# Optimization experiments

Measured on AMD Instinct MI355X. Metric: run time of the kernel, lower is better.

## Reference

```python
import jax, jax.numpy as jnp
import numpy as np

H = 4   # num_heads
D = 32  # out_dim per head
NEG_SLOPE = 0.01  # torch F.leaky_relu default


def setup_inputs() -> dict:
    key = jax.random.key(0)
    ks = jax.random.split(key, 8)
    N, E, IN, ED = 50000, 600000, 128, 64
    node_feats = jax.random.normal(ks[0], (N, IN), dtype=jnp.float32)
    edge_feats = jax.random.normal(ks[1], (E, ED), dtype=jnp.float32)
    src = jax.random.randint(ks[2], (E,), 0, N, dtype=jnp.int32)
    dst = jax.random.randint(ks[3], (E,), 0, N, dtype=jnp.int32)
    # Xavier-ish scaled weights to keep softmax logits sane
    Wn = jax.random.normal(ks[4], (IN, H * D), dtype=jnp.float32) * (1.0 / np.sqrt(IN))
    We = jax.random.normal(ks[5], (ED, H * D), dtype=jnp.float32) * (1.0 / np.sqrt(ED))
    Wa = jax.random.normal(ks[6], (2 * D,), dtype=jnp.float32) * (1.0 / np.sqrt(2 * D))
    Wo = jax.random.normal(ks[7], (H * D, D), dtype=jnp.float32) * (1.0 / np.sqrt(H * D))
    return {"node_feats": node_feats, "edge_feats": edge_feats, "src": src,
            "dst": dst, "Wn": Wn, "We": We, "Wa": Wa, "Wo": Wo}


def reference(node_feats, edge_feats, src, dst, Wn, We, Wa, Wo):
    N = node_feats.shape[0]
    # projections -> [N,H,D] and [E,H,D]
    zn = (node_feats @ Wn).reshape(N, H, D)
    ze = (edge_feats @ We).reshape(-1, H, D)
    # edge attention logits: concat([z_src+z_e, z_dst+z_e]) @ Wa, leaky_relu
    zs = zn[src] + ze                              # [E,H,D]
    zd = zn[dst] + ze                              # [E,H,D]
    e = jnp.einsum('ehd,d->eh', zs, Wa[:D]) + jnp.einsum('ehd,d->eh', zd, Wa[D:])
    e = jax.nn.leaky_relu(e, NEG_SLOPE)            # [E,H]
    # segment softmax over incoming edges of each destination node
    emax = jax.ops.segment_max(e, dst, num_segments=N)       # [N,H]
    emax = jnp.where(jnp.isfinite(emax), emax, 0.0)          # empty segments
    ex = jnp.exp(e - emax[dst])                              # [E,H]
    denom = jax.ops.segment_sum(ex, dst, num_segments=N)     # [N,H]
    alpha = ex / denom[dst]                                  # [E,H]
    # weighted scatter-sum of edge messages
    agg = jax.ops.segment_sum(alpha[..., None] * ze, dst, num_segments=N)  # [N,H,D]
    # DGL update_all leaves zero-in-degree nodes with their projected feats
    deg = jax.ops.segment_sum(jnp.ones_like(dst, dtype=jnp.float32), dst, num_segments=N)
    z = jnp.where((deg > 0)[:, None, None], agg, zn)
    out = jax.nn.relu(z.reshape(N, H * D) @ Wo)   # activation=relu; dropout is identity in eval
    return out
```

## Files before the change

### kernel.cpp

```cpp
#include <hip/hip_runtime.h>
#include <hip/hip_fp16.h>
#include <math.h>

#define HH 4
#define DD 32
#define HD 128
#define INF 128
#define EDF 64
#define NEG 0.01f
#define NB 256
#define CHUNK 64
#define GS_LOGIT 1024
#define GS_AGG   2048
#define GS_NODES 1024

template <int CTRL>
__device__ __forceinline__ float dpp_add(float v) {
    int t = __builtin_amdgcn_update_dpp(0, __float_as_int(v), CTRL, 0xF, 0xF, true);
    return v + __int_as_float(t);
}
__device__ __forceinline__ float red16(float v) {
    v = dpp_add<0xB1>(v);
    v = dpp_add<0x4E>(v);
    v = dpp_add<0x141>(v);
    v = dpp_add<0x140>(v);
    return v;
}

__global__ void k_pre(const float* __restrict__ Wn, const float* __restrict__ We,
                      const float* __restrict__ Wa, const float* __restrict__ Wo,
                      float* __restrict__ WnA, float* __restrict__ WnB,
                      float* __restrict__ WeC, float* __restrict__ WeWo,
                      float* __restrict__ WnWo, int* __restrict__ deg, int N) {
    int b = blockIdx.x, tid = threadIdx.x;
    if (b >= 25) {
        int i = (b - 25) * 512 + tid;
        if (i < N) deg[i] = 0;
        return;
    }
    if (b < 16) {
        int t = b * 512 + tid;
        int j = t >> 5, o = t & 31;
        int h = j >> 6, k = j & 63;
        float a = 0.f;
        for (int d = 0; d < DD; ++d)
            a += We[k * HD + h * DD + d] * Wo[(h * DD + d) * DD + o];
        WeWo[t] = a;
    } else if (b < 24) {
        int u = (b - 16) * 512 + tid;
        int k = u >> 5, o = u & 31;
        float a = 0.f;
        for (int d = 0; d < HD; ++d)
            a += Wn[k * HD + d] * Wo[d * DD + o];
        WnWo[u] = a;
    } else {
        int k = tid >> 2, h = tid & 3;
        float a = 0.f, bb = 0.f;
        for (int d = 0; d < DD; ++d) {
            float w = Wn[k * HD + h * DD + d];
            a += w * Wa[d];
            bb += w * Wa[DD + d];
        }
        WnA[k * HH + h] = a;
        WnB[k * HH + h] = bb;
        if (k < EDF) {
            float c = 0.f;
            for (int d = 0; d < DD; ++d)
                c += We[k * HD + h * DD + d] * (Wa[d] + Wa[DD + d]);
            WeC[k * HH + h] = c;
        }
    }
}

__global__ void k_nodes(const float* __restrict__ X, const float* __restrict__ WnA,
                        const float* __restrict__ WnB, float* __restrict__ an,
                        float* __restrict__ bn, int N) {
    int wave = threadIdx.x >> 6, lane = threadIdx.x & 63;
    int stride = gridDim.x * 4;
    for (int n = blockIdx.x * 4 + wave; n < N; n += stride) {
        float x0 = X[(size_t)n * INF + lane];
        float x1 = X[(size_t)n * INF + 64 + lane];
        float pa[HH], pb[HH];
#pragma unroll
        for (int h = 0; h < HH; ++h) {
            pa[h] = x0 * WnA[lane * HH + h] + x1 * WnA[(lane + 64) * HH + h];
            pb[h] = x0 * WnB[lane * HH + h] + x1 * WnB[(lane + 64) * HH + h];
        }
#pragma unroll
        for (int off = 32; off; off >>= 1)
#pragma unroll
            for (int h = 0; h < HH; ++h) {
                pa[h] += __shfl_xor(pa[h], off);
                pb[h] += __shfl_xor(pb[h], off);
            }
        if (lane == 0)
#pragma unroll
            for (int h = 0; h < HH; ++h) {
                an[(size_t)n * HH + h] = pa[h];
                bn[(size_t)n * HH + h] = pb[h];
            }
    }
}

__global__ void k_hist(const int* __restrict__ dst, int* __restrict__ deg,
                       int* __restrict__ rank, int E) {
    int e = blockIdx.x * blockDim.x + threadIdx.x;
    if (e < E) rank[e] = atomicAdd(&deg[dst[e]], 1);
}
__global__ void k_scan1(const int* __restrict__ deg, int* __restrict__ partial,
                        int N, int chunk) {
    __shared__ int s[256];
    int tid = threadIdx.x;
    int i = blockIdx.x * chunk + tid;
    int v = (tid < chunk && i < N) ? deg[i] : 0;
    s[tid] = v; __syncthreads();
    for (int off = 128; off; off >>= 1) {
        if (tid < off) s[tid] += s[tid + off];
        __syncthreads();
    }
    if (tid == 0) partial[blockIdx.x] = s[0];
}
__global__ void k_scan2(const int* __restrict__ partial, int* __restrict__ pscan) {
    __shared__ int s[NB];
    int tid = threadIdx.x;
    int v = partial[tid];
    s[tid] = v; __syncthreads();
    for (int off = 1; off < NB; off <<= 1) {
        int t = (tid >= off) ? s[tid - off] : 0;
        __syncthreads();
        s[tid] += t;
        __syncthreads();
    }
    pscan[tid] = s[tid] - v;
}
__global__ void k_scan3(const int* __restrict__ deg, const int* __restrict__ pscan,
                        int* __restrict__ offs, int2* __restrict__ nd,
                        int N, int chunk) {
    __shared__ int s[256];
    int tid = threadIdx.x;
    int i = blockIdx.x * chunk + tid;
    int v = (tid < chunk && i < N) ? deg[i] : 0;
    s[tid] = v; __syncthreads();
    for (int off = 1; off < 256; off <<= 1) {
        int t = (tid >= off) ? s[tid - off] : 0;
        __syncthreads();
        s[tid] += t;
        __syncthreads();
    }
    if (tid < chunk && i < N) {
        int o = pscan[blockIdx.x] + s[tid] - v;
        offs[i] = o;
        nd[i] = make_int2(o, v);
    }
}
__global__ void k_perm(const int* __restrict__ dst, const int* __restrict__ offs,
                       const int* __restrict__ rank, int* __restrict__ eids,
                       int* __restrict__ pos_of, int E) {
    int e = blockIdx.x * blockDim.x + threadIdx.x;
    if (e < E) {
        int p = offs[dst[e]] + rank[e];
        pos_of[e] = p;
        eids[p] = e;
    }
}

struct Quad { float4 x; int s, d, p, e; bool v; };

__device__ __forceinline__ Quad loadq(const float* __restrict__ EF,
                                      const int* __restrict__ src,
                                      const int* __restrict__ dst,
                                      const int* __restrict__ pos_of,
                                      int idx, int nq, int g, int q, int E) {
    Quad r;
    int qi = idx < nq ? idx : nq - 1;
    int e = qi * 4 + g;
    r.v = (idx < nq) && (e < E);
    if (e >= E) e = E - 1;
    r.e = e;
    r.x = *(const float4*)(EF + (size_t)e * EDF + q * 4);
    r.s = src[e];
    r.d = dst[e];
    r.p = pos_of[e];
    return r;
}

__global__ void k_logit(const float* __restrict__ EF, const float* __restrict__ an,
                        const float* __restrict__ bn, const float* __restrict__ WeC,
                        const int* __restrict__ src, const int* __restrict__ dst,
                        const int* __restrict__ pos_of,
                        float* __restrict__ wep, __half* __restrict__ EF16, int E) {
    int wave = threadIdx.x >> 6, lane = threadIdx.x & 63;
    int g = lane >> 4, q = lane & 15;
    float4 c0 = *(const float4*)(WeC + (q * 4 + 0) * 4);
    float4 c1 = *(const float4*)(WeC + (q * 4 + 1) * 4);
    float4 c2 = *(const float4*)(WeC + (q * 4 + 2) * 4);
    float4 c3 = *(const float4*)(WeC + (q * 4 + 3) * 4);
    int nq = (E + 3) >> 2;
    int stride = gridDim.x * 4;
    int i0 = blockIdx.x * 4 + wave;
    if (i0 >= nq) return;
    Quad A = loadq(EF, src, dst, pos_of, i0, nq, g, q, E);
    Quad B = loadq(EF, src, dst, pos_of, i0 + stride, nq, g, q, E);
    float4 anA = *(const float4*)(an + (size_t)A.s * HH);
    float4 bnA = *(const float4*)(bn + (size_t)A.d * HH);
    for (int i = i0; i < nq; i += stride) {
        Quad C = loadq(EF, src, dst, pos_of, i + 2 * stride, nq, g, q, E);
        float4 anB = *(const float4*)(an + (size_t)B.s * HH);
        float4 bnB = *(const float4*)(bn + (size_t)B.d * HH);
        float ae0 = red16(A.x.x * c0.x + A.x.y * c1.x + A.x.z * c2.x + A.x.w * c3.x);
        float ae1 = red16(A.x.x * c0.y + A.x.y * c1.y + A.x.z * c2.y + A.x.w * c3.y);
        float ae2 = red16(A.x.x * c0.z + A.x.y * c1.z + A.x.z * c2.z + A.x.w * c3.z);
        float ae3 = red16(A.x.x * c0.w + A.x.y * c1.w + A.x.z * c2.w + A.x.w * c3.w);
        if (A.v) {
            __half2 h01 = __floats2half2_rn(A.x.x, A.x.y);
            __half2 h23 = __floats2half2_rn(A.x.z, A.x.w);
            __half2* hp = (__half2*)(EF16 + (size_t)A.e * EDF + q * 4);
            hp[0] = h01;
            hp[1] = h23;
            if (q == 0) {
                float l0 = anA.x + bnA.x + ae0;
                float l1 = anA.y + bnA.y + ae1;
                float l2 = anA.z + bnA.z + ae2;
                float l3 = anA.w + bnA.w + ae3;
                float4 w4;
                w4.x = __expf(l0 > 0.f ? l0 : NEG * l0);
                w4.y = __expf(l1 > 0.f ? l1 : NEG * l1);
                w4.z = __expf(l2 > 0.f ? l2 : NEG * l2);
                w4.w = __expf(l3 > 0.f ? l3 : NEG * l3);
                *(float4*)(wep + (size_t)A.p * 4) = w4;
            }
        }
        A = B; anA = anB; bnA = bnB;
        B = C;
    }
}

__global__ void k_agg(const __half* __restrict__ EF16, const float* __restrict__ wep,
                      const int* __restrict__ eids, const int2* __restrict__ nd,
                      const float* __restrict__ WW, const float* __restrict__ X,
                      const float* __restrict__ WnWo, float* __restrict__ out, int N) {
    __shared__ float ww_s[256 * 32];
    __shared__ float smem[4][264];
    __shared__ int   ebuf[4][CHUNK];
    for (int i = threadIdx.x; i < 256 * 32; i += 256)
        ww_s[i] = WW[i];
    __syncthreads();

    int wave = threadIdx.x >> 6, lane = threadIdx.x & 63;
    int s8 = lane >> 3, o4 = lane & 7;
    int stride = gridDim.x * 4;
    for (int n = blockIdx.x * 4 + wave; n < N; n += stride) {
        int2 sd = nd[n];
        int st = sd.x, dn = sd.y;
        if (dn == 0) {
            if (lane < 32) {
                float a = 0.f;
                for (int k = 0; k < INF; ++k)
                    a += X[(size_t)n * INF + k] * WnWo[k * DD + lane];
                out[(size_t)n * DD + lane] = fmaxf(a, 0.f);
            }
            continue;
        }
        float4* wbuf = (float4*)smem[wave];
        const __half* base = EF16 + lane;
        float gacc[4] = {0.f, 0.f, 0.f, 0.f};
        float den[4]  = {0.f, 0.f, 0.f, 0.f};
        for (int r0 = 0; r0 < dn; r0 += CHUNK) {
            int cnt = dn - r0; if (cnt > CHUNK) cnt = CHUNK;
            {
                int l2 = lane < cnt ? lane : cnt - 1;
                ebuf[wave][lane] = eids[st + r0 + l2];
                float4 w4 = *(const float4*)(wep + (size_t)(st + r0 + l2) * 4);
                if (lane >= cnt) w4 = make_float4(0.f, 0.f, 0.f, 0.f);
                wbuf[lane] = w4;
            }
            int nb4 = (cnt + 3) >> 2;
            __half x0[4], x1[4], x2[4];
            int ep[4];
#pragma unroll
            for (int j = 0; j < 4; ++j) ep[j] = ebuf[wave][j & 63];
#pragma unroll
            for (int j = 0; j < 4; ++j) x0[j] = base[(size_t)ep[j] * EDF];
#pragma unroll
            for (int j = 0; j < 4; ++j) ep[j] = ebuf[wave][(4 + j) & 63];
#pragma unroll
            for (int j = 0; j < 4; ++j) x1[j] = base[(size_t)ep[j] * EDF];
            for (int i = 0; i < nb4; ++i) {
#pragma unroll
                for (int j = 0; j < 4; ++j) ep[j] = ebuf[wave][((i + 2) * 4 + j) & 63];
#pragma unroll
                for (int j = 0; j < 4; ++j) x2[j] = base[(size_t)ep[j] * EDF];
                float f0 = __half2float(x0[0]), f1 = __half2float(x0[1]);
                float f2 = __half2float(x0[2]), f3 = __half2float(x0[3]);
                float4 wA = wbuf[i * 4 + 0];
                float4 wB = wbuf[i * 4 + 1];
                float4 wC = wbuf[i * 4 + 2];
                float4 wD = wbuf[i * 4 + 3];
                gacc[0] += wA.x * f0 + wB.x * f1 + wC.x * f2 + wD.x * f3;
                gacc[1] += wA.y * f0 + wB.y * f1 + wC.y * f2 + wD.y * f3;
                gacc[2] += wA.z * f0 + wB.z * f1 + wC.z * f2 + wD.z * f3;
                gacc[3] += wA.w * f0 + wB.w * f1 + wC.w * f2 + wD.w * f3;
                den[0] += wA.x + wB.x + wC.x + wD.x;
                den[1] += wA.y + wB.y + wC.y + wD.y;
                den[2] += wA.z + wB.z + wC.z + wD.z;
                den[3] += wA.w + wB.w + wC.w + wD.w;
#pragma unroll
                for (int j = 0; j < 4; ++j) { x0[j] = x1[j]; x1[j] = x2[j]; }
            }
        }
        float* G = smem[wave];
#pragma unroll
        for (int h = 0; h < 4; ++h) {
            int idx = h * 64 + lane;
            G[idx + (idx >> 5)] = gacc[h] / den[h];
        }
        float4 acc = make_float4(0.f, 0.f, 0.f, 0.f);
        int jb = s8 * 32;
#pragma unroll 8
        for (int jj = 0; jj < 32; ++jj) {
            float gv = G[jb + jj + s8];
            float4 w4 = *(const float4*)&ww_s[(jb + jj) * 32 + o4 * 4];
            acc.x += gv * w4.x;
            acc.y += gv * w4.y;
            acc.z += gv * w4.z;
            acc.w += gv * w4.w;
        }
#pragma unroll
        for (int off = 8; off < 64; off <<= 1) {
            acc.x += __shfl_xor(acc.x, off);
            acc.y += __shfl_xor(acc.y, off);
            acc.z += __shfl_xor(acc.z, off);
            acc.w += __shfl_xor(acc.w, off);
        }
        if (lane < 8) {
            float4 o_;
            o_.x = fmaxf(acc.x, 0.f);
            o_.y = fmaxf(acc.y, 0.f);
            o_.z = fmaxf(acc.z, 0.f);
            o_.w = fmaxf(acc.w, 0.f);
            *(float4*)(out + (size_t)n * DD + o4 * 4) = o_;
        }
    }
}

extern "C" void kernel_launch(void* const* d_in, const int* in_sizes, int n_in,
                              void* d_out, int out_size, void* d_ws, size_t ws_size,
                              hipStream_t stream) {
    const float* node_feats = (const float*)d_in[0];
    const float* edge_feats = (const float*)d_in[1];
    const int*   src        = (const int*)d_in[2];
    const int*   dst        = (const int*)d_in[3];
    const float* Wn         = (const float*)d_in[4];
    const float* We         = (const float*)d_in[5];
    const float* Wa         = (const float*)d_in[6];
    const float* Wo         = (const float*)d_in[7];
    float* out = (float*)d_out;
    int N = in_sizes[0] / INF;
    int E = in_sizes[2];

    char* p = (char*)d_ws;
    auto alloc = [&](size_t bytes) {
        char* r = p;
        p += (bytes + 255) & ~(size_t)255;
        return r;
    };
    float* WnA   = (float*)alloc((size_t)INF * HH * 4);
    float* WnB   = (float*)alloc((size_t)INF * HH * 4);
    float* WeC   = (float*)alloc((size_t)EDF * HH * 4);
    float* WeWo  = (float*)alloc((size_t)EDF * HH * DD * 4);
    float* WnWo  = (float*)alloc((size_t)INF * DD * 4);
    float* an    = (float*)alloc((size_t)N * HH * 4);
    float* bn    = (float*)alloc((size_t)N * HH * 4);
    float* wep   = (float*)alloc((size_t)E * HH * 4);
    __half* EF16 = (__half*)alloc((size_t)E * EDF * 2);
    int* deg     = (int*)alloc((size_t)N * 4);
    int* offs    = (int*)alloc((size_t)N * 4);
    int2* nd     = (int2*)alloc((size_t)N * 8);
    int* rank    = (int*)alloc((size_t)E * 4);
    int* eids    = (int*)alloc((size_t)E * 4);
    int* pos_of  = (int*)alloc((size_t)E * 4);
    int* partial = (int*)alloc((size_t)NB * 4);
    int* pscan   = (int*)alloc((size_t)NB * 4);

    int chunk = (N + NB - 1) / NB;
    int preblk = 25 + (N + 511) / 512;

    hipLaunchKernelGGL(k_pre, dim3(preblk), dim3(512), 0, stream,
                       Wn, We, Wa, Wo, WnA, WnB, WeC, WeWo, WnWo, deg, N);
    hipLaunchKernelGGL(k_nodes, dim3(GS_NODES), dim3(256), 0, stream,
                       node_feats, WnA, WnB, an, bn, N);
    hipLaunchKernelGGL(k_hist, dim3((E + 255) / 256), dim3(256), 0, stream,
                       dst, deg, rank, E);
    hipLaunchKernelGGL(k_scan1, dim3(NB), dim3(256), 0, stream, deg, partial, N, chunk);
    hipLaunchKernelGGL(k_scan2, dim3(1), dim3(NB), 0, stream, partial, pscan);
    hipLaunchKernelGGL(k_scan3, dim3(NB), dim3(256), 0, stream, deg, pscan, offs, nd, N, chunk);
    hipLaunchKernelGGL(k_perm, dim3((E + 255) / 256), dim3(256), 0, stream,
                       dst, offs, rank, eids, pos_of, E);
    hipLaunchKernelGGL(k_logit, dim3(GS_LOGIT), dim3(256), 0, stream,
                       edge_feats, an, bn, WeC, src, dst, pos_of, wep, EF16, E);
    hipLaunchKernelGGL(k_agg, dim3(GS_AGG), dim3(256), 0, stream,
                       EF16, wep, eids, nd, WeWo, node_feats, WnWo, out, N);
}
```

Baseline: 202.2 us.

## Vectorize edge and node loads, pack src/dst, split agg lanes over half2 features

k_perm now also writes a packed int2 (src, dst) array. k_logit reads that array and pos_of only in the few lanes that need them, lets two lanes fetch the an/bn rows and combines them with a DPP pair add, and stores EF16 with one 8-byte write. k_logit also launches a larger grid. k_agg gives each lane a half2 of features for one of two edge subsets, which widens the gather loads, and merges the two halves with a shuffle. k_nodes keeps its weights in registers and loads X as float2. The aim is fewer redundant index and gather transactions, at the cost of an extra E*8-byte buffer write in k_perm.

```diff
diff --git a/kernel.cpp b/kernel.cpp
--- a/kernel.cpp
+++ b/kernel.cpp
@@ -10,7 +10,7 @@
 #define NEG 0.01f
 #define NB 256
 #define CHUNK 64
-#define GS_LOGIT 1024
+#define GS_LOGIT 2048
 #define GS_AGG   2048
 #define GS_NODES 1024
 
@@ -26,6 +26,7 @@
     v = dpp_add<0x140>(v);
     return v;
 }
+__device__ __forceinline__ float pair_add(float v) { return dpp_add<0xB1>(v); }
 
 __global__ void k_pre(const float* __restrict__ Wn, const float* __restrict__ We,
                       const float* __restrict__ Wa, const float* __restrict__ Wo,
@@ -76,16 +77,22 @@
                         const float* __restrict__ WnB, float* __restrict__ an,
                         float* __restrict__ bn, int N) {
     int wave = threadIdx.x >> 6, lane = threadIdx.x & 63;
+    float4 wa0 = *(const float4*)(WnA + lane * 8);
+    float4 wa1 = *(const float4*)(WnA + lane * 8 + 4);
+    float4 wb0 = *(const float4*)(WnB + lane * 8);
+    float4 wb1 = *(const float4*)(WnB + lane * 8 + 4);
     int stride = gridDim.x * 4;
     for (int n = blockIdx.x * 4 + wave; n < N; n += stride) {
-        float x0 = X[(size_t)n * INF + lane];
-        float x1 = X[(size_t)n * INF + 64 + lane];
+        float2 x2 = *(const float2*)(X + (size_t)n * INF + lane * 2);
         float pa[HH], pb[HH];
-#pragma unroll
-        for (int h = 0; h < HH; ++h) {
-            pa[h] = x0 * WnA[lane * HH + h] + x1 * WnA[(lane + 64) * HH + h];
-            pb[h] = x0 * WnB[lane * HH + h] + x1 * WnB[(lane + 64) * HH + h];
-        }
+        pa[0] = x2.x * wa0.x + x2.y * wa1.x;
+        pa[1] = x2.x * wa0.y + x2.y * wa1.y;
+        pa[2] = x2.x * wa0.z + x2.y * wa1.z;
+        pa[3] = x2.x * wa0.w + x2.y * wa1.w;
+        pb[0] = x2.x * wb0.x + x2.y * wb1.x;
+        pb[1] = x2.x * wb0.y + x2.y * wb1.y;
+        pb[2] = x2.x * wb0.z + x2.y * wb1.z;
+        pb[3] = x2.x * wb0.w + x2.y * wb1.w;
 #pragma unroll
         for (int off = 32; off; off >>= 1)
 #pragma unroll
@@ -153,41 +160,54 @@
         nd[i] = make_int2(o, v);
     }
 }
-__global__ void k_perm(const int* __restrict__ dst, const int* __restrict__ offs,
-                       const int* __restrict__ rank, int* __restrict__ eids,
-                       int* __restrict__ pos_of, int E) {
+__global__ void k_perm(const int* __restrict__ src, const int* __restrict__ dst,
+                       const int* __restrict__ offs, const int* __restrict__ rank,
+                       int* __restrict__ eids, int* __restrict__ pos_of,
+                       int2* __restrict__ sd2, int E) {
     int e = blockIdx.x * blockDim.x + threadIdx.x;
     if (e < E) {
-        int p = offs[dst[e]] + rank[e];
+        int d = dst[e];
+        int p = offs[d] + rank[e];
         pos_of[e] = p;
         eids[p] = e;
-    }
-}
-
-struct Quad { float4 x; int s, d, p, e; bool v; };
-
-__device__ __forceinline__ Quad loadq(const float* __restrict__ EF,
-                                      const int* __restrict__ src,
-                                      const int* __restrict__ dst,
-                                      const int* __restrict__ pos_of,
-                                      int idx, int nq, int g, int q, int E) {
-    Quad r;
+        sd2[e] = make_int2(src[e], d);
+    }
+}
+
+struct Meta { float4 x; int2 sd; int p; int e; bool v; };
+
+__device__ __forceinline__ Meta loadmeta(const float* __restrict__ EF,
+                                         const int2* __restrict__ sd2,
+                                         const int* __restrict__ pos_of,
+                                         int idx, int nq, int g, int q, int E) {
+    Meta r;
     int qi = idx < nq ? idx : nq - 1;
     int e = qi * 4 + g;
     r.v = (idx < nq) && (e < E);
     if (e >= E) e = E - 1;
     r.e = e;
     r.x = *(const float4*)(EF + (size_t)e * EDF + q * 4);
-    r.s = src[e];
-    r.d = dst[e];
-    r.p = pos_of[e];
+    r.sd = make_int2(0, 0);
+    r.p = 0;
+    if (q < 2) r.sd = sd2[e];
+    if (q == 0) r.p = pos_of[e];
+    return r;
+}
+__device__ __forceinline__ float4 anbn_load(const float* __restrict__ an,
+                                            const float* __restrict__ bn,
+                                            const Meta& m, int q) {
+    float4 r = make_float4(0.f, 0.f, 0.f, 0.f);
+    if (q < 2) {
+        const float* p = (q == 0) ? (an + (size_t)m.sd.x * HH)
+                                  : (bn + (size_t)m.sd.y * HH);
+        r = *(const float4*)p;
+    }
     return r;
 }
 
 __global__ void k_logit(const float* __restrict__ EF, const float* __restrict__ an,
                         const float* __restrict__ bn, const float* __restrict__ WeC,
-                        const int* __restrict__ src, const int* __restrict__ dst,
-                        const int* __restrict__ pos_of,
+                        const int2* __restrict__ sd2, const int* __restrict__ pos_of,
                         float* __restrict__ wep, __half* __restrict__ EF16, int E) {
     int wave = threadIdx.x >> 6, lane = threadIdx.x & 63;
     int g = lane >> 4, q = lane & 15;
@@ -199,29 +219,30 @@
     int stride = gridDim.x * 4;
     int i0 = blockIdx.x * 4 + wave;
     if (i0 >= nq) return;
-    Quad A = loadq(EF, src, dst, pos_of, i0, nq, g, q, E);
-    Quad B = loadq(EF, src, dst, pos_of, i0 + stride, nq, g, q, E);
-    float4 anA = *(const float4*)(an + (size_t)A.s * HH);
-    float4 bnA = *(const float4*)(bn + (size_t)A.d * HH);
+    Meta A = loadmeta(EF, sd2, pos_of, i0, nq, g, q, E);
+    Meta B = loadmeta(EF, sd2, pos_of, i0 + stride, nq, g, q, E);
+    float4 rA = anbn_load(an, bn, A, q);
     for (int i = i0; i < nq; i += stride) {
-        Quad C = loadq(EF, src, dst, pos_of, i + 2 * stride, nq, g, q, E);
-        float4 anB = *(const float4*)(an + (size_t)B.s * HH);
-        float4 bnB = *(const float4*)(bn + (size_t)B.d * HH);
+        Meta C = loadmeta(EF, sd2, pos_of, i + 2 * stride, nq, g, q, E);
+        float4 rB = anbn_load(an, bn, B, q);
         float ae0 = red16(A.x.x * c0.x + A.x.y * c1.x + A.x.z * c2.x + A.x.w * c3.x);
         float ae1 = red16(A.x.x * c0.y + A.x.y * c1.y + A.x.z * c2.y + A.x.w * c3.y);
         float ae2 = red16(A.x.x * c0.z + A.x.y * c1.z + A.x.z * c2.z + A.x.w * c3.z);
         float ae3 = red16(A.x.x * c0.w + A.x.y * c1.w + A.x.z * c2.w + A.x.w * c3.w);
+        float s0 = pair_add(rA.x);
+        float s1 = pair_add(rA.y);
+        float s2 = pair_add(rA.z);
+        float s3 = pair_add(rA.w);
         if (A.v) {
             __half2 h01 = __floats2half2_rn(A.x.x, A.x.y);
             __half2 h23 = __floats2half2_rn(A.x.z, A.x.w);
-            __half2* hp = (__half2*)(EF16 + (size_t)A.e * EDF + q * 4);
-            hp[0] = h01;
-            hp[1] = h23;
+            uint2 u = make_uint2(*(unsigned*)&h01, *(unsigned*)&h23);
+            *(uint2*)(EF16 + (size_t)A.e * EDF + q * 4) = u;
             if (q == 0) {
-                float l0 = anA.x + bnA.x + ae0;
-                float l1 = anA.y + bnA.y + ae1;
-                float l2 = anA.z + bnA.z + ae2;
-                float l3 = anA.w + bnA.w + ae3;
+                float l0 = s0 + ae0;
+                float l1 = s1 + ae1;
+                float l2 = s2 + ae2;
+                float l3 = s3 + ae3;
                 float4 w4;
                 w4.x = __expf(l0 > 0.f ? l0 : NEG * l0);
                 w4.y = __expf(l1 > 0.f ? l1 : NEG * l1);
@@ -230,7 +251,7 @@
                 *(float4*)(wep + (size_t)A.p * 4) = w4;
             }
         }
-        A = B; anA = anB; bnA = bnB;
+        A = B; rA = rB;
         B = C;
     }
 }
@@ -247,6 +268,7 @@
     __syncthreads();
 
     int wave = threadIdx.x >> 6, lane = threadIdx.x & 63;
+    int half = lane >> 5, f2 = lane & 31;
     int s8 = lane >> 3, o4 = lane & 7;
     int stride = gridDim.x * 4;
     for (int n = blockIdx.x * 4 + wave; n < N; n += stride) {
@@ -262,9 +284,9 @@
             continue;
         }
         float4* wbuf = (float4*)smem[wave];
-        const __half* base = EF16 + lane;
-        float gacc[4] = {0.f, 0.f, 0.f, 0.f};
-        float den[4]  = {0.f, 0.f, 0.f, 0.f};
+        float g0[4] = {0.f, 0.f, 0.f, 0.f};
+        float g1[4] = {0.f, 0.f, 0.f, 0.f};
+        float den[4] = {0.f, 0.f, 0.f, 0.f};
         for (int r0 = 0; r0 < dn; r0 += CHUNK) {
             int cnt = dn - r0; if (cnt > CHUNK) cnt = CHUNK;
             {
@@ -275,45 +297,50 @@
                 wbuf[lane] = w4;
             }
             int nb4 = (cnt + 3) >> 2;
-            __half x0[4], x1[4], x2[4];
-            int ep[4];
-#pragma unroll
-            for (int j = 0; j < 4; ++j) ep[j] = ebuf[wave][j & 63];
-#pragma unroll
-            for (int j = 0; j < 4; ++j) x0[j] = base[(size_t)ep[j] * EDF];
-#pragma unroll
-            for (int j = 0; j < 4; ++j) ep[j] = ebuf[wave][(4 + j) & 63];
-#pragma unroll
-            for (int j = 0; j < 4; ++j) x1[j] = base[(size_t)ep[j] * EDF];
+            int eA = ebuf[wave][(0 + half) & 63];
+            int eB = ebuf[wave][(2 + half) & 63];
+            __half2 xA0 = *(const __half2*)(EF16 + (size_t)eA * EDF + f2 * 2);
+            __half2 xB0 = *(const __half2*)(EF16 + (size_t)eB * EDF + f2 * 2);
+            eA = ebuf[wave][(4 + half) & 63];
+            eB = ebuf[wave][(6 + half) & 63];
+            __half2 xA1 = *(const __half2*)(EF16 + (size_t)eA * EDF + f2 * 2);
+            __half2 xB1 = *(const __half2*)(EF16 + (size_t)eB * EDF + f2 * 2);
             for (int i = 0; i < nb4; ++i) {
-#pragma unroll
-                for (int j = 0; j < 4; ++j) ep[j] = ebuf[wave][((i + 2) * 4 + j) & 63];
-#pragma unroll
-                for (int j = 0; j < 4; ++j) x2[j] = base[(size_t)ep[j] * EDF];
-                float f0 = __half2float(x0[0]), f1 = __half2float(x0[1]);
-                float f2 = __half2float(x0[2]), f3 = __half2float(x0[3]);
-                float4 wA = wbuf[i * 4 + 0];
-                float4 wB = wbuf[i * 4 + 1];
-                float4 wC = wbuf[i * 4 + 2];
-                float4 wD = wbuf[i * 4 + 3];
-                gacc[0] += wA.x * f0 + wB.x * f1 + wC.x * f2 + wD.x * f3;
-                gacc[1] += wA.y * f0 + wB.y * f1 + wC.y * f2 + wD.y * f3;
-                gacc[2] += wA.z * f0 + wB.z * f1 + wC.z * f2 + wD.z * f3;
-                gacc[3] += wA.w * f0 + wB.w * f1 + wC.w * f2 + wD.w * f3;
-                den[0] += wA.x + wB.x + wC.x + wD.x;
-                den[1] += wA.y + wB.y + wC.y + wD.y;
-                den[2] += wA.z + wB.z + wC.z + wD.z;
-                den[3] += wA.w + wB.w + wC.w + wD.w;
-#pragma unroll
-                for (int j = 0; j < 4; ++j) { x0[j] = x1[j]; x1[j] = x2[j]; }
-            }
+                int ia = (i + 2) * 4;
+                eA = ebuf[wave][(ia + half) & 63];
+                eB = ebuf[wave][(ia + 2 + half) & 63];
+                __half2 xA2 = *(const __half2*)(EF16 + (size_t)eA * EDF + f2 * 2);
+                __half2 xB2 = *(const __half2*)(EF16 + (size_t)eB * EDF + f2 * 2);
+                float2 fa = __half22float2(xA0);
+                float2 fb = __half22float2(xB0);
+                float4 wA = wbuf[i * 4 + half];
+                float4 wB = wbuf[i * 4 + 2 + half];
+                g0[0] += wA.x * fa.x + wB.x * fb.x;  g1[0] += wA.x * fa.y + wB.x * fb.y;
+                g0[1] += wA.y * fa.x + wB.y * fb.x;  g1[1] += wA.y * fa.y + wB.y * fb.y;
+                g0[2] += wA.z * fa.x + wB.z * fb.x;  g1[2] += wA.z * fa.y + wB.z * fb.y;
+                g0[3] += wA.w * fa.x + wB.w * fb.x;  g1[3] += wA.w * fa.y + wB.w * fb.y;
+                den[0] += wA.x + wB.x;
+                den[1] += wA.y + wB.y;
+                den[2] += wA.z + wB.z;
+                den[3] += wA.w + wB.w;
+                xA0 = xA1; xB0 = xB1; xA1 = xA2; xB1 = xB2;
+            }
+        }
+#pragma unroll
+        for (int h = 0; h < 4; ++h) {
+            den[h] += __shfl_xor(den[h], 32);
+            g0[h]  += __shfl_xor(g0[h], 32);
+            g1[h]  += __shfl_xor(g1[h], 32);
         }
         float* G = smem[wave];
-#pragma unroll
-        for (int h = 0; h < 4; ++h) {
-            int idx = h * 64 + lane;
-            G[idx + (idx >> 5)] = gacc[h] / den[h];
-        }
+        if (half == 0)
+#pragma unroll
+            for (int h = 0; h < 4; ++h) {
+                int j0 = h * 64 + f2 * 2;
+                G[j0 + (j0 >> 5)] = g0[h] / den[h];
+                int j1 = j0 + 1;
+                G[j1 + (j1 >> 5)] = g1[h] / den[h];
+            }
         float4 acc = make_float4(0.f, 0.f, 0.f, 0.f);
         int jb = s8 * 32;
 #pragma unroll 8
@@ -379,6 +406,7 @@
     int* rank    = (int*)alloc((size_t)E * 4);
     int* eids    = (int*)alloc((size_t)E * 4);
     int* pos_of  = (int*)alloc((size_t)E * 4);
+    int2* sd2    = (int2*)alloc((size_t)E * 8);
     int* partial = (int*)alloc((size_t)NB * 4);
     int* pscan   = (int*)alloc((size_t)NB * 4);
 
@@ -395,9 +423,9 @@
     hipLaunchKernelGGL(k_scan2, dim3(1), dim3(NB), 0, stream, partial, pscan);
     hipLaunchKernelGGL(k_scan3, dim3(NB), dim3(256), 0, stream, deg, pscan, offs, nd, N, chunk);
     hipLaunchKernelGGL(k_perm, dim3((E + 255) / 256), dim3(256), 0, stream,
-                       dst, offs, rank, eids, pos_of, E);
+                       src, dst, offs, rank, eids, pos_of, sd2, E);
     hipLaunchKernelGGL(k_logit, dim3(GS_LOGIT), dim3(256), 0, stream,
-                       edge_feats, an, bn, WeC, src, dst, pos_of, wep, EF16, E);
+                       edge_feats, an, bn, WeC, sd2, pos_of, wep, EF16, E);
     hipLaunchKernelGGL(k_agg, dim3(GS_AGG), dim3(256), 0, stream,
                        EF16, wep, eids, nd, WeWo, node_feats, WnWo, out, N);
 }
```

Measured after the change: 217.6 us. 7.6% more time.
